# Kernel optimization log

Hardware: AMD Instinct MI355X
Metric: run time of the kernel (lower is better)

The kernel has to match this reference:

```python
import jax, jax.numpy as jnp
import numpy as np

N, E, IN, HID, H, L, G = 20000, 320000, 128, 64, 4, 3, 128

def setup_inputs() -> dict:
    key = jax.random.key(0)
    ks = jax.random.split(key, 14)
    x = jax.random.normal(ks[0], (N, IN), dtype=jnp.float32)
    edge_index = jax.random.randint(ks[1], (2, E), 0, N, dtype=jnp.int64)
    batch = jnp.sort(jax.random.randint(ks[2], (N,), 0, G, dtype=jnp.int64))
    s_in = 1.0 / np.sqrt(IN)
    s_h = 1.0 / np.sqrt(HID)
    lin_W = jax.random.normal(ks[3], (IN, HID), jnp.float32) * s_in
    lin_b = jax.random.normal(ks[4], (HID,), jnp.float32) * 0.02
    Wq = jax.random.normal(ks[5], (L, HID, H * HID), jnp.float32) * s_h
    bq = jax.random.normal(ks[6], (L, H * HID), jnp.float32) * 0.02
    Wk = jax.random.normal(ks[7], (L, HID, H * HID), jnp.float32) * s_h
    bk = jax.random.normal(ks[8], (L, H * HID), jnp.float32) * 0.02
    Wv = jax.random.normal(ks[9], (L, HID, H * HID), jnp.float32) * s_h
    bv = jax.random.normal(ks[10], (L, H * HID), jnp.float32) * 0.02
    Ws = jax.random.normal(ks[11], (L, HID, HID), jnp.float32) * s_h
    bs = jax.random.normal(ks[12], (L, HID), jnp.float32) * 0.02
    return {"x": x, "edge_index": edge_index, "batch": batch,
            "lin_W": lin_W, "lin_b": lin_b, "Wq": Wq, "bq": bq,
            "Wk": Wk, "bk": bk, "Wv": Wv, "bv": bv, "Ws": Ws, "bs": bs}

def _transformer_conv(h, src, dst, Wq, bq, Wk, bk, Wv, bv, Ws, bs):
    # PyG TransformerConv(hid, hid, heads=H, concat=False), beta=False, root_weight=True
    n = h.shape[0]
    C = HID  # per-head dim
    q = (h @ Wq + bq).reshape(n, H, C)
    k = (h @ Wk + bk).reshape(n, H, C)
    v = (h @ Wv + bv).reshape(n, H, C)
    # per-edge attention logits: q_i . k_j / sqrt(C), i=dst (target), j=src
    alpha = jnp.einsum('ehc,ehc->eh', q[dst], k[src]) * (1.0 / np.sqrt(C))  # [E,H]
    # segment softmax over edges grouped by target node
    amax = jax.ops.segment_max(alpha, dst, num_segments=n)  # [N,H]
    amax = jnp.where(jnp.isfinite(amax), amax, 0.0)
    ex = jnp.exp(alpha - amax[dst])
    denom = jax.ops.segment_sum(ex, dst, num_segments=n)
    a = ex / jnp.maximum(denom[dst], 1e-16)  # [E,H]
    msg = a[:, :, None] * v[src]  # [E,H,C]
    agg = jax.ops.segment_sum(msg.reshape(-1, H * C), dst, num_segments=n)
    out = agg.reshape(n, H, C).mean(axis=1)  # concat=False -> head mean
    return out + h @ Ws + bs  # root/skip connection

def reference(x, edge_index, batch, lin_W, lin_b, Wq, bq, Wk, bk, Wv, bv, Ws, bs):
    src, dst = edge_index[0], edge_index[1]
    h = x @ lin_W + lin_b  # [N, HID]; dropout inactive in eval
    for l in range(L):
        h = jax.nn.relu(_transformer_conv(h, src, dst, Wq[l], bq[l], Wk[l], bk[l],
                                          Wv[l], bv[l], Ws[l], bs[l]))
    # global_add_pool: sum node features per graph
    return jax.ops.segment_sum(h, batch, num_segments=G)  # [G, HID]
```

## Files before the change

kernel.cpp:

```cpp
#include <hip/hip_runtime.h>
#include <math.h>

#define N_NODES 20000
#define N_EDGES 320000
#define DIM_IN 128
#define HID 64
#define HEADS 4
#define LAYERS 3
#define GRAPHS 128
#define QSS 320

typedef unsigned short ushort;
typedef ushort ushort8 __attribute__((ext_vector_type(8)));

__device__ __forceinline__ float bf2f(ushort u) {
    return __uint_as_float(((unsigned int)u) << 16);
}
__device__ __forceinline__ ushort f2bf(float f) {
    unsigned int b = __float_as_uint(f);
    return (ushort)((b + 0x7FFFu + ((b >> 16) & 1u)) >> 16);
}


__global__ void hist_kernel(const int* __restrict__ dst, int* __restrict__ counts, int n) {
    int e = blockIdx.x * 256 + threadIdx.x;
    if (e < n) atomicAdd(&counts[dst[e]], 1);
}

__global__ __launch_bounds__(256) void blocksum_kernel(const int* __restrict__ counts,
                                                       int* __restrict__ bsum, int n) {
    int i = blockIdx.x * 256 + threadIdx.x;
    int v = (i < n) ? counts[i] : 0;
    int lane = threadIdx.x & 63, wave = threadIdx.x >> 6;
#pragma unroll
    for (int off = 32; off >= 1; off >>= 1) v += __shfl_xor(v, off);
    __shared__ int ws[4];
    if (lane == 0) ws[wave] = v;
    __syncthreads();
    if (threadIdx.x == 0) bsum[blockIdx.x] = ws[0] + ws[1] + ws[2] + ws[3];
}

__global__ __launch_bounds__(128) void scanb_kernel(const int* __restrict__ bsum,
                                                    int* __restrict__ bexcl, int nb) {
    int tid = threadIdx.x;
    int v = (tid < nb) ? bsum[tid] : 0;
    int lane = tid & 63, wave = tid >> 6;
    int s = v;
#pragma unroll
    for (int off = 1; off < 64; off <<= 1) {
        int t = __shfl_up(s, off);
        if (lane >= off) s += t;
    }
    __shared__ int w0sum;
    if (tid == 63) w0sum = s;
    __syncthreads();
    int excl = s - v + (wave ? w0sum : 0);
    if (tid < nb) bexcl[tid] = excl;
}

__global__ __launch_bounds__(256) void expand_kernel(const int* __restrict__ counts,
                                                     const int* __restrict__ bexcl,
                                                     int* __restrict__ offs,
                                                     int* __restrict__ cursor, int n) {
    int i = blockIdx.x * 256 + threadIdx.x;
    int v = (i < n) ? counts[i] : 0;
    int lane = threadIdx.x & 63, wave = threadIdx.x >> 6;
    int s = v;
#pragma unroll
    for (int off = 1; off < 64; off <<= 1) {
        int t = __shfl_up(s, off);
        if (lane >= off) s += t;
    }
    __shared__ int wsum[4];
    if (lane == 63) wsum[wave] = s;
    __syncthreads();
    int add = bexcl[blockIdx.x];
    for (int w = 0; w < wave; ++w) add += wsum[w];
    int excl = add + s - v;
    if (i < n) { offs[i] = excl; cursor[i] = excl; }
    if (i == 0) offs[n] = N_EDGES;
}

__global__ void scatter_kernel(const int* __restrict__ src, const int* __restrict__ dst,
                               int* __restrict__ cursor, int* __restrict__ csr, int n) {
    int e = blockIdx.x * 256 + threadIdx.x;
    if (e < n) {
        int d = dst[e];
        int pos = atomicAdd(&cursor[d], 1);
        csr[pos] = src[e];
    }
}


__global__ __launch_bounds__(256) void lin_kernel(const float* __restrict__ x,
                                                  const float* __restrict__ W,
                                                  const float* __restrict__ b,
                                                  float* __restrict__ h0) {
    __shared__ float xt[32][DIM_IN];
    int tx = threadIdx.x;
    int row0 = blockIdx.x * 32;
    for (int idx = tx; idx < 32 * DIM_IN; idx += 256) {
        int r = idx / DIM_IN, c = idx % DIM_IN;
        xt[r][c] = x[(size_t)(row0 + r) * DIM_IN + c];
    }
    __syncthreads();
    int col = tx & 63;
    int sub = tx >> 6;
    float acc[8];
#pragma unroll
    for (int r = 0; r < 8; ++r) acc[r] = 0.f;
    for (int k = 0; k < DIM_IN; k += 4) {
        float w0 = W[k * HID + col];
        float w1 = W[(k + 1) * HID + col];
        float w2 = W[(k + 2) * HID + col];
        float w3 = W[(k + 3) * HID + col];
#pragma unroll
        for (int r = 0; r < 8; ++r) {
            const float4 hv = *(const float4*)&xt[r * 4 + sub][k];
            acc[r] += hv.x * w0 + hv.y * w1 + hv.z * w2 + hv.w * w3;
        }
    }
    float bias = b[col];
#pragma unroll
    for (int r = 0; r < 8; ++r) {
        int row = row0 + r * 4 + sub;
        h0[(size_t)row * HID + col] = acc[r] + bias;
    }
}


__global__ __launch_bounds__(256) void proj_kernel(const float* __restrict__ h,
                                                   const float* __restrict__ Wq, const float* __restrict__ bq,
                                                   const float* __restrict__ Wk, const float* __restrict__ bk,
                                                   const float* __restrict__ Wv, const float* __restrict__ bv,
                                                   const float* __restrict__ Ws, const float* __restrict__ bs,
                                                   float* __restrict__ qs,
                                                   ushort* __restrict__ kvpack) {
    __shared__ float ht[16][HID];
    int tx = threadIdx.x;
    int row0 = blockIdx.x * 16;
    for (int idx = tx; idx < 16 * HID; idx += 256) {
        ht[idx >> 6][idx & 63] = h[(size_t)(row0 + (idx >> 6)) * HID + (idx & 63)];
    }
    __syncthreads();
    const bool do_s = (tx < 64);
    float accq[16], acck[16], accv[16], accs[16];
#pragma unroll
    for (int r = 0; r < 16; ++r) { accq[r] = 0.f; acck[r] = 0.f; accv[r] = 0.f; accs[r] = 0.f; }

    for (int k = 0; k < HID; k += 4) {
        float wq0 = Wq[(size_t)k * 256 + tx];
        float wq1 = Wq[(size_t)(k + 1) * 256 + tx];
        float wq2 = Wq[(size_t)(k + 2) * 256 + tx];
        float wq3 = Wq[(size_t)(k + 3) * 256 + tx];
        float wk0 = Wk[(size_t)k * 256 + tx];
        float wk1 = Wk[(size_t)(k + 1) * 256 + tx];
        float wk2 = Wk[(size_t)(k + 2) * 256 + tx];
        float wk3 = Wk[(size_t)(k + 3) * 256 + tx];
        float wv0 = Wv[(size_t)k * 256 + tx];
        float wv1 = Wv[(size_t)(k + 1) * 256 + tx];
        float wv2 = Wv[(size_t)(k + 2) * 256 + tx];
        float wv3 = Wv[(size_t)(k + 3) * 256 + tx];
        float ws0 = 0.f, ws1 = 0.f, ws2 = 0.f, ws3 = 0.f;
        if (do_s) {
            ws0 = Ws[(size_t)k * 64 + tx];
            ws1 = Ws[(size_t)(k + 1) * 64 + tx];
            ws2 = Ws[(size_t)(k + 2) * 64 + tx];
            ws3 = Ws[(size_t)(k + 3) * 64 + tx];
        }
#pragma unroll
        for (int r = 0; r < 16; ++r) {
            const float4 hv = *(const float4*)&ht[r][k];
            accq[r] += hv.x * wq0 + hv.y * wq1 + hv.z * wq2 + hv.w * wq3;
            acck[r] += hv.x * wk0 + hv.y * wk1 + hv.z * wk2 + hv.w * wk3;
            accv[r] += hv.x * wv0 + hv.y * wv1 + hv.z * wv2 + hv.w * wv3;
        }
        if (do_s) {
#pragma unroll
            for (int r = 0; r < 16; ++r) {
                const float4 hv = *(const float4*)&ht[r][k];
                accs[r] += hv.x * ws0 + hv.y * ws1 + hv.z * ws2 + hv.w * ws3;
            }
        }
    }

    float biasq = bq[tx], biask = bk[tx], biasv = bv[tx];
    int hh = tx >> 6, c = tx & 63;
    int posk = (hh * 16 + (c >> 2)) * 8 + (c & 3);
    int posv = posk + 4;
#pragma unroll
    for (int r = 0; r < 16; ++r) {
        size_t row = row0 + r;
        qs[row * QSS + tx] = accq[r] + biasq;
        kvpack[row * 512 + posk] = f2bf(acck[r] + biask);
        kvpack[row * 512 + posv] = f2bf(accv[r] + biasv);
    }
    if (do_s) {
        float biass = bs[tx];
#pragma unroll
        for (int r = 0; r < 16; ++r)
            qs[(size_t)(row0 + r) * QSS + 256 + tx] = accs[r] + biass;
    }
}


__global__ __launch_bounds__(256) void edge_kernel(const float* __restrict__ qs,
                                                   const ushort8* __restrict__ kvp,
                                                   const int* __restrict__ offs,
                                                   const int* __restrict__ csr,
                                                   float* __restrict__ hout) {
    int wave = threadIdx.x >> 6;
    int lane = threadIdx.x & 63;
    int node = blockIdx.x * 4 + wave;
    if (node >= N_NODES) return;
    int hh = lane >> 4;
    int cb = (lane & 15) * 4;

    const float* nb = qs + (size_t)node * QSS;
    float4 q = *(const float4*)(nb + hh * 64 + cb);

    float m = -INFINITY, l = 0.f;
    float4 acc = make_float4(0.f, 0.f, 0.f, 0.f);

    int e0 = offs[node], e1 = offs[node + 1];
    int cnt = e1 - e0;

    ushort8 cur = (ushort8)(0);
    ushort8 nxt = (ushort8)(0);
    if (cnt > 0) cur = kvp[(size_t)csr[e0] * 64 + lane];
    if (cnt > 1) nxt = kvp[(size_t)csr[e0 + 1] * 64 + lane];

    for (int i = 0; i < cnt; ++i) {
        ushort8 u = cur;
        cur = nxt;
        if (i + 2 < cnt) nxt = kvp[(size_t)csr[e0 + i + 2] * 64 + lane];

        float p = q.x * bf2f(u[0]) + q.y * bf2f(u[1]) + q.z * bf2f(u[2]) + q.w * bf2f(u[3]);
        p += __shfl_xor(p, 1);
        p += __shfl_xor(p, 2);
        p += __shfl_xor(p, 4);
        p += __shfl_xor(p, 8);
        float alpha = p * 0.125f;
        float nm = fmaxf(m, alpha);
        float sc = __expf(m - nm);
        float pe = __expf(alpha - nm);
        l = l * sc + pe;
        acc.x = acc.x * sc + pe * bf2f(u[4]);
        acc.y = acc.y * sc + pe * bf2f(u[5]);
        acc.z = acc.z * sc + pe * bf2f(u[6]);
        acc.w = acc.w * sc + pe * bf2f(u[7]);
        m = nm;
    }

    float inv = (l > 0.f) ? (1.f / l) : 0.f;
    float4 r;
    r.x = acc.x * inv;
    r.y = acc.y * inv;
    r.z = acc.z * inv;
    r.w = acc.w * inv;
    r.x += __shfl_xor(r.x, 16); r.x += __shfl_xor(r.x, 32);
    r.y += __shfl_xor(r.y, 16); r.y += __shfl_xor(r.y, 32);
    r.z += __shfl_xor(r.z, 16); r.z += __shfl_xor(r.z, 32);
    r.w += __shfl_xor(r.w, 16); r.w += __shfl_xor(r.w, 32);

    if (hh == 0) {
        float4 s = *(const float4*)(nb + 256 + cb);
        float4 o;
        o.x = fmaxf(r.x * 0.25f + s.x, 0.f);
        o.y = fmaxf(r.y * 0.25f + s.y, 0.f);
        o.z = fmaxf(r.z * 0.25f + s.z, 0.f);
        o.w = fmaxf(r.w * 0.25f + s.w, 0.f);
        *(float4*)(hout + (size_t)node * HID + cb) = o;
    }
}


__global__ __launch_bounds__(256) void pool_kernel(const float* __restrict__ h,
                                                   const int* __restrict__ batch,
                                                   float* __restrict__ out) {
    int g = blockIdx.x;
    int lo = 0, hi = N_NODES;
    while (lo < hi) { int mid = (lo + hi) >> 1; if (batch[mid] < g) lo = mid + 1; else hi = mid; }
    int start = lo;
    hi = N_NODES;
    while (lo < hi) { int mid = (lo + hi) >> 1; if (batch[mid] < g + 1) lo = mid + 1; else hi = mid; }
    int end = lo;
    int c = threadIdx.x & 63;
    int sub = threadIdx.x >> 6;
    float acc = 0.f;
    for (int i = start + sub; i < end; i += 4) acc += h[(size_t)i * HID + c];
    __shared__ float lds[4][64];
    lds[sub][c] = acc;
    __syncthreads();
    if (sub == 0) out[g * HID + c] = lds[0][c] + lds[1][c] + lds[2][c] + lds[3][c];
}


extern "C" void kernel_launch(void* const* d_in, const int* in_sizes, int n_in,
                              void* d_out, int out_size, void* d_ws, size_t ws_size,
                              hipStream_t stream) {
    const float* x    = (const float*)d_in[0];
    const int*   edge = (const int*)d_in[1];
    const int*   batch= (const int*)d_in[2];
    const float* linW = (const float*)d_in[3];
    const float* linb = (const float*)d_in[4];
    const float* Wq   = (const float*)d_in[5];
    const float* bq   = (const float*)d_in[6];
    const float* Wk   = (const float*)d_in[7];
    const float* bk   = (const float*)d_in[8];
    const float* Wv   = (const float*)d_in[9];
    const float* bv   = (const float*)d_in[10];
    const float* Ws   = (const float*)d_in[11];
    const float* bs   = (const float*)d_in[12];
    float* out = (float*)d_out;

    const int* src = edge;
    const int* dst = edge + N_EDGES;

    float* h0  = (float*)d_ws;
    float* h1  = h0 + (size_t)N_NODES * HID;
    float* qs  = h1 + (size_t)N_NODES * HID;
    ushort* kvpack = (ushort*)(qs + (size_t)N_NODES * QSS);
    int* counts = (int*)(kvpack + (size_t)N_NODES * 512);
    int* offs   = counts + N_NODES;
    int* cursor = offs + N_NODES + 1;
    int* csr    = cursor + N_NODES;
    int* bsum   = csr + N_EDGES;
    int* bexcl  = bsum + 128;

    const int NB = (N_NODES + 255) / 256;

    hipMemsetAsync(counts, 0, N_NODES * sizeof(int), stream);
    hist_kernel<<<(N_EDGES + 255) / 256, 256, 0, stream>>>(dst, counts, N_EDGES);
    blocksum_kernel<<<NB, 256, 0, stream>>>(counts, bsum, N_NODES);
    scanb_kernel<<<1, 128, 0, stream>>>(bsum, bexcl, NB);
    expand_kernel<<<NB, 256, 0, stream>>>(counts, bexcl, offs, cursor, N_NODES);
    scatter_kernel<<<(N_EDGES + 255) / 256, 256, 0, stream>>>(src, dst, cursor, csr, N_EDGES);

    lin_kernel<<<N_NODES / 32, 256, 0, stream>>>(x, linW, linb, h0);

    float* hc = h0;
    float* hn = h1;
    for (int l = 0; l < LAYERS; ++l) {
        proj_kernel<<<N_NODES / 16, 256, 0, stream>>>(hc,
            Wq + (size_t)l * HID * 256, bq + (size_t)l * 256,
            Wk + (size_t)l * HID * 256, bk + (size_t)l * 256,
            Wv + (size_t)l * HID * 256, bv + (size_t)l * 256,
            Ws + (size_t)l * HID * 64,  bs + (size_t)l * 64,
            qs, kvpack);
        edge_kernel<<<N_NODES / 4, 256, 0, stream>>>(qs, (const ushort8*)kvpack, offs, csr, hn);
        float* t = hc; hc = hn; hn = t;
    }

    pool_kernel<<<GRAPHS, 256, 0, stream>>>(hc, batch, out);
}
```

Measured before the change: 445.9 us.

## Use bf16 MFMA for fused QKV/skip projection with pre-transposed weights

```diff
diff --git a/kernel.cpp b/kernel.cpp
--- a/kernel.cpp
+++ b/kernel.cpp
@@ -12,6 +12,8 @@
 
 typedef unsigned short ushort;
 typedef ushort ushort8 __attribute__((ext_vector_type(8)));
+typedef short short8 __attribute__((ext_vector_type(8)));
+typedef float f32x4 __attribute__((ext_vector_type(4)));
 
 __device__ __forceinline__ float bf2f(ushort u) {
     return __uint_as_float(((unsigned int)u) << 16);
@@ -129,77 +131,93 @@
 }
 
 
-__global__ __launch_bounds__(256) void proj_kernel(const float* __restrict__ h,
-                                                   const float* __restrict__ Wq, const float* __restrict__ bq,
+__global__ __launch_bounds__(256) void wcvt_kernel(const float* __restrict__ Wq, const float* __restrict__ bq,
                                                    const float* __restrict__ Wk, const float* __restrict__ bk,
                                                    const float* __restrict__ Wv, const float* __restrict__ bv,
                                                    const float* __restrict__ Ws, const float* __restrict__ bs,
+                                                   ushort* __restrict__ Wt, float* __restrict__ bias_cat) {
+    int idx = blockIdx.x * 256 + threadIdx.x;
+    if (idx < 832 * 64) {
+        int j = idx >> 6, k = idx & 63;
+        float w;
+        if (j < 256)      w = Wq[(size_t)k * 256 + j];
+        else if (j < 512) w = Wk[(size_t)k * 256 + (j - 256)];
+        else if (j < 768) w = Wv[(size_t)k * 256 + (j - 512)];
+        else              w = Ws[(size_t)k * 64 + (j - 768)];
+        Wt[idx] = f2bf(w);
+    }
+    if (idx < 832) {
+        float b;
+        if (idx < 256)      b = bq[idx];
+        else if (idx < 512) b = bk[idx - 256];
+        else if (idx < 768) b = bv[idx - 512];
+        else                b = bs[idx - 768];
+        bias_cat[idx] = b;
+    }
+}
+
+
+__global__ __launch_bounds__(512) void proj_kernel(const float* __restrict__ h,
+                                                   const ushort* __restrict__ Wt,
+                                                   const float* __restrict__ bias_cat,
                                                    float* __restrict__ qs,
                                                    ushort* __restrict__ kvpack) {
-    __shared__ float ht[16][HID];
-    int tx = threadIdx.x;
-    int row0 = blockIdx.x * 16;
-    for (int idx = tx; idx < 16 * HID; idx += 256) {
-        ht[idx >> 6][idx & 63] = h[(size_t)(row0 + (idx >> 6)) * HID + (idx & 63)];
-    }
-    __syncthreads();
-    const bool do_s = (tx < 64);
-    float accq[16], acck[16], accv[16], accs[16];
-#pragma unroll
-    for (int r = 0; r < 16; ++r) { accq[r] = 0.f; acck[r] = 0.f; accv[r] = 0.f; accs[r] = 0.f; }
-
-    for (int k = 0; k < HID; k += 4) {
-        float wq0 = Wq[(size_t)k * 256 + tx];
-        float wq1 = Wq[(size_t)(k + 1) * 256 + tx];
-        float wq2 = Wq[(size_t)(k + 2) * 256 + tx];
-        float wq3 = Wq[(size_t)(k + 3) * 256 + tx];
-        float wk0 = Wk[(size_t)k * 256 + tx];
-        float wk1 = Wk[(size_t)(k + 1) * 256 + tx];
-        float wk2 = Wk[(size_t)(k + 2) * 256 + tx];
-        float wk3 = Wk[(size_t)(k + 3) * 256 + tx];
-        float wv0 = Wv[(size_t)k * 256 + tx];
-        float wv1 = Wv[(size_t)(k + 1) * 256 + tx];
-        float wv2 = Wv[(size_t)(k + 2) * 256 + tx];
-        float wv3 = Wv[(size_t)(k + 3) * 256 + tx];
-        float ws0 = 0.f, ws1 = 0.f, ws2 = 0.f, ws3 = 0.f;
-        if (do_s) {
-            ws0 = Ws[(size_t)k * 64 + tx];
-            ws1 = Ws[(size_t)(k + 1) * 64 + tx];
-            ws2 = Ws[(size_t)(k + 2) * 64 + tx];
-            ws3 = Ws[(size_t)(k + 3) * 64 + tx];
+    int tid = threadIdx.x;
+    int w = tid >> 6, l = tid & 63;
+    int r0 = blockIdx.x * 32 + (w & 1) * 16;
+    int c0 = (w >> 1) * 208;
+    int row = r0 + (l & 15);
+    int koff = (l >> 4) * 8;
+
+    short8 a[2];
+#pragma unroll
+    for (int m = 0; m < 2; ++m) {
+        const float* hp = h + (size_t)row * HID + m * 32 + koff;
+        float4 f0 = *(const float4*)hp;
+        float4 f1 = *(const float4*)(hp + 4);
+        ushort8 u;
+        u[0] = f2bf(f0.x); u[1] = f2bf(f0.y); u[2] = f2bf(f0.z); u[3] = f2bf(f0.w);
+        u[4] = f2bf(f1.x); u[5] = f2bf(f1.y); u[6] = f2bf(f1.z); u[7] = f2bf(f1.w);
+        a[m] = __builtin_bit_cast(short8, u);
+    }
+
+    f32x4 acc[13];
+#pragma unroll
+    for (int t = 0; t < 13; ++t) acc[t] = (f32x4){0.f, 0.f, 0.f, 0.f};
+
+    const ushort* wb = Wt + ((size_t)(c0 + (l & 15))) * HID + koff;
+#pragma unroll
+    for (int t = 0; t < 13; ++t) {
+        short8 b0 = *(const short8*)(wb + (size_t)t * 16 * HID);
+        short8 b1 = *(const short8*)(wb + (size_t)t * 16 * HID + 32);
+        acc[t] = __builtin_amdgcn_mfma_f32_16x16x32_bf16(a[0], b0, acc[t], 0, 0, 0);
+        acc[t] = __builtin_amdgcn_mfma_f32_16x16x32_bf16(a[1], b1, acc[t], 0, 0, 0);
+    }
+
+    int colbase = c0 + (l & 15);
+    int rbase = r0 + ((l >> 4) << 2);
+#pragma unroll
+    for (int t = 0; t < 13; ++t) {
+        int j = colbase + t * 16;
+        float bias = bias_cat[j];
+        if (j < 256) {
+#pragma unroll
+            for (int i = 0; i < 4; ++i)
+                qs[(size_t)(rbase + i) * QSS + j] = acc[t][i] + bias;
+        } else if (j < 768) {
+            int ck = j - 256;
+            int isv = ck >> 8;
+            int ch = ck & 255;
+            int hh2 = ch >> 6, c = ch & 63;
+            int pos = (hh2 * 16 + (c >> 2)) * 8 + isv * 4 + (c & 3);
+#pragma unroll
+            for (int i = 0; i < 4; ++i)
+                kvpack[(size_t)(rbase + i) * 512 + pos] = f2bf(acc[t][i] + bias);
+        } else {
+#pragma unroll
+            for (int i = 0; i < 4; ++i)
+                qs[(size_t)(rbase + i) * QSS + 256 + (j - 768)] = acc[t][i] + bias;
         }
-#pragma unroll
-        for (int r = 0; r < 16; ++r) {
-            const float4 hv = *(const float4*)&ht[r][k];
-            accq[r] += hv.x * wq0 + hv.y * wq1 + hv.z * wq2 + hv.w * wq3;
-            acck[r] += hv.x * wk0 + hv.y * wk1 + hv.z * wk2 + hv.w * wk3;
-            accv[r] += hv.x * wv0 + hv.y * wv1 + hv.z * wv2 + hv.w * wv3;
-        }
-        if (do_s) {
-#pragma unroll
-            for (int r = 0; r < 16; ++r) {
-                const float4 hv = *(const float4*)&ht[r][k];
-                accs[r] += hv.x * ws0 + hv.y * ws1 + hv.z * ws2 + hv.w * ws3;
-            }
-        }
-    }
-
-    float biasq = bq[tx], biask = bk[tx], biasv = bv[tx];
-    int hh = tx >> 6, c = tx & 63;
-    int posk = (hh * 16 + (c >> 2)) * 8 + (c & 3);
-    int posv = posk + 4;
-#pragma unroll
-    for (int r = 0; r < 16; ++r) {
-        size_t row = row0 + r;
-        qs[row * QSS + tx] = accq[r] + biasq;
-        kvpack[row * 512 + posk] = f2bf(acck[r] + biask);
-        kvpack[row * 512 + posv] = f2bf(accv[r] + biasv);
-    }
-    if (do_s) {
-        float biass = bs[tx];
-#pragma unroll
-        for (int r = 0; r < 16; ++r)
-            qs[(size_t)(row0 + r) * QSS + 256 + tx] = accs[r] + biass;
     }
 }
 
@@ -327,6 +345,8 @@
     int* csr    = cursor + N_NODES;
     int* bsum   = csr + N_EDGES;
     int* bexcl  = bsum + 128;
+    ushort* Wt  = (ushort*)(bexcl + 128);
+    float* bias_cat = (float*)(Wt + 832 * 64);
 
     const int NB = (N_NODES + 255) / 256;
 
@@ -342,12 +362,13 @@
     float* hc = h0;
     float* hn = h1;
     for (int l = 0; l < LAYERS; ++l) {
-        proj_kernel<<<N_NODES / 16, 256, 0, stream>>>(hc,
+        wcvt_kernel<<<(832 * 64 + 255) / 256, 256, 0, stream>>>(
             Wq + (size_t)l * HID * 256, bq + (size_t)l * 256,
             Wk + (size_t)l * HID * 256, bk + (size_t)l * 256,
             Wv + (size_t)l * HID * 256, bv + (size_t)l * 256,
             Ws + (size_t)l * HID * 64,  bs + (size_t)l * 64,
-            qs, kvpack);
+            Wt, bias_cat);
+        proj_kernel<<<N_NODES / 32, 512, 0, stream>>>(hc, Wt, bias_cat, qs, kvpack);
         edge_kernel<<<N_NODES / 4, 256, 0, stream>>>(qs, (const ushort8*)kvpack, offs, csr, hn);
         float* t = hc; hc = hn; hn = t;
     }
```

Measured after the change: 404.3 us. 9.3% less time.
